# Kernel tuning notes

Measured on AMD Instinct MI355X. Metric: run time of the kernel, lower is better.

## Reference

```python
import jax, jax.numpy as jnp
import numpy as np

# Straight-through sign: forward = sign (with sign(0)=+1), backward = identity clipped to |x|<=1.
# Used both for weight binarization (BinaryLinearLayer) and StepActivationFunction.
@jax.custom_vjp
def ste_sign(x):
    return jnp.where(x >= 0, 1.0, -1.0).astype(x.dtype)

def _ste_fwd(x):
    return ste_sign(x), x

def _ste_bwd(x, g):
    return (g * (jnp.abs(x) <= 1.0).astype(g.dtype),)

ste_sign.defvjp(_ste_fwd, _ste_bwd)

def binary_linear(x, w):
    # BinaryLinearLayer: matmul against sign-binarized weights, no bias.
    return x @ ste_sign(w).T


def setup_inputs() -> dict:
    key = jax.random.key(0)
    ks = jax.random.split(key, 5)
    B = 65536
    x = jax.random.normal(ks[0], (B, 784), dtype=jnp.float32)
    w1 = jax.random.normal(ks[1], (256, 784), dtype=jnp.float32) * 0.1
    w2 = jax.random.normal(ks[2], (128, 256), dtype=jnp.float32) * 0.1
    w3 = jax.random.normal(ks[3], (32, 128), dtype=jnp.float32) * 0.1
    w4 = jax.random.normal(ks[4], (10, 32), dtype=jnp.float32) * 0.1
    return {"x": x, "w1": w1, "w2": w2, "w3": w3, "w4": w4}


def reference(x, w1, w2, w3, w4):
    h = x.reshape(-1, 28 * 28)                 # [B, 784]
    h = ste_sign(binary_linear(h, w1))         # [B, 256]
    h = ste_sign(binary_linear(h, w2))         # [B, 128]
    h = ste_sign(binary_linear(h, w3))         # [B, 32]
    return binary_linear(h, w4)                # [B, 10] logits, no final step
```

## Files before the change

### kernel.cpp

```cpp
#include <hip/hip_runtime.h>
#include <stdint.h>

typedef __bf16 bf16;
typedef bf16 bf16x8 __attribute__((ext_vector_type(8)));
typedef float f32x4 __attribute__((ext_vector_type(4)));

#define B_ROWS   65536
#define K1       784
#define CAPW     64
#define NWAVES   4096

#define CNT_OFF  0
#define LIST_OFF 16384
#define S1F_OFF  1064960
#define W2P_OFF  1474560
#define W3P_OFF  1478656
#define W4P_OFF  1479168
#define H1P_OFF  1479680

#define AS1C(p) ((const __attribute__((address_space(1))) void*)(p))
#define AS3(p)  ((__attribute__((address_space(3))) void*)(p))

__global__ __launch_bounds__(256) void prep_kernel(
    const float* __restrict__ w1, const float* __restrict__ w2,
    const float* __restrict__ w3, const float* __restrict__ w4,
    bf16* __restrict__ s1f, uint32_t* __restrict__ w2p,
    uint32_t* __restrict__ w3p, uint32_t* __restrict__ w4p) {
  int gid = blockIdx.x * 256 + threadIdx.x;
  {
    int j = gid & 7, l = (gid >> 3) & 63, t = (gid >> 9) & 15, s = gid >> 13;
    int fr = l & 15, fg = l >> 4;
    int n = t * 16 + fr;
    int k = s * 32 + fg * 8 + j;
    bf16 v = (bf16)0.0f;
    if (k < K1) v = (w1[n * K1 + k] >= 0.0f) ? (bf16)1.0f : (bf16)-1.0f;
    s1f[gid] = v;
  }
  if (gid < 1024) {
    int j = gid >> 3, w = gid & 7;
    uint32_t bits = 0;
    for (int i = 0; i < 32; ++i)
      bits |= (w2[j * 256 + w * 32 + i] >= 0.0f ? 1u : 0u) << i;
    w2p[gid] = bits;
  }
  if (gid < 128) {
    int j = gid >> 2, w = gid & 3;
    uint32_t bits = 0;
    for (int i = 0; i < 32; ++i)
      bits |= (w3[j * 128 + w * 32 + i] >= 0.0f ? 1u : 0u) << i;
    w3p[gid] = bits;
  }
  if (gid < 16) {
    uint32_t bits = 0;
    if (gid < 10)
      for (int i = 0; i < 32; ++i)
        bits |= (w4[gid * 32 + i] >= 0.0f ? 1u : 0u) << i;
    w4p[gid] = bits;
  }
}

__global__ __launch_bounds__(256, 4) void gemm1_kernel(
    const float* __restrict__ x, const bf16* __restrict__ s1f,
    uint8_t* __restrict__ h1b, uint32_t* __restrict__ cntArr,
    uint32_t* __restrict__ list) {
  __shared__ __align__(16) bf16 Bs[2][8192];

  const int tid = threadIdx.x;
  const int lane = tid & 63;
  const int wid = tid >> 6;
  const int fr = lane & 15, fg = lane >> 4;
  const int m0 = blockIdx.x * 64 + wid * 16;
  const int waveId = blockIdx.x * 4 + wid;

  f32x4 acc[16];
#pragma unroll
  for (int j = 0; j < 16; ++j) acc[j] = (f32x4){0.f, 0.f, 0.f, 0.f};

  const float* xp0 = x + (size_t)(m0 + fr) * K1 + fg * 8;

  float4 ar[2][2];

#define STAGE_B(buf_, t_)                                                      \
  {                                                                            \
    _Pragma("unroll") for (int c = 0; c < 4; ++c)                              \
        __builtin_amdgcn_global_load_lds(                                      \
            AS1C(s1f + ((size_t)(t_) * 16 + wid * 4 + c) * 512 + lane * 8),    \
            AS3(&Bs[buf_][(wid * 4 + c) * 512]), 16, 0, 0);                    \
  }

#define LOAD_A(par_, t_)                                                       \
  {                                                                            \
    ar[par_][0] = *(const float4*)(xp0 + (t_) * 32);                           \
    ar[par_][1] = *(const float4*)(xp0 + (t_) * 32 + 4);                       \
  }

#define LOAD_A24(par_)                                                         \
  {                                                                            \
    float4 z = make_float4(0.f, 0.f, 0.f, 0.f);                                \
    if (fg < 2) {                                                              \
      ar[par_][0] = *(const float4*)(xp0 + 24 * 32);                           \
      ar[par_][1] = *(const float4*)(xp0 + 24 * 32 + 4);                       \
    } else {                                                                   \
      ar[par_][0] = z; ar[par_][1] = z;                                        \
    }                                                                          \
  }

#define STEP(t_, cur_, nxt_, PF_)                                              \
  {                                                                            \
    if ((PF_) == 1) LOAD_A(nxt_, (t_) + 1)                                     \
    else if ((PF_) == 2) LOAD_A24(nxt_)                                        \
    if ((PF_) != 0) STAGE_B((cur_) ^ 1, (t_) + 1)                              \
    bf16x8 ah, al;                                                             \
    {                                                                          \
      float4 v0 = ar[cur_][0], v1 = ar[cur_][1];                               \
      bf16 h0 = (bf16)v0.x, h1 = (bf16)v0.y, h2 = (bf16)v0.z, h3 = (bf16)v0.w; \
      bf16 h4 = (bf16)v1.x, h5 = (bf16)v1.y, h6 = (bf16)v1.z, h7 = (bf16)v1.w; \
      bf16 l0 = (bf16)(v0.x - (float)h0), l1 = (bf16)(v0.y - (float)h1);       \
      bf16 l2 = (bf16)(v0.z - (float)h2), l3 = (bf16)(v0.w - (float)h3);       \
      bf16 l4 = (bf16)(v1.x - (float)h4), l5 = (bf16)(v1.y - (float)h5);       \
      bf16 l6 = (bf16)(v1.z - (float)h6), l7 = (bf16)(v1.w - (float)h7);       \
      ah = (bf16x8){h0, h1, h2, h3, h4, h5, h6, h7};                           \
      al = (bf16x8){l0, l1, l2, l3, l4, l5, l6, l7};                           \
    }                                                                          \
    _Pragma("unroll") for (int jg = 0; jg < 4; ++jg) {                         \
      bf16x8 b0 = *(const bf16x8*)&Bs[cur_][(jg * 4 + 0) * 512 + lane * 8];    \
      bf16x8 b1 = *(const bf16x8*)&Bs[cur_][(jg * 4 + 1) * 512 + lane * 8];    \
      bf16x8 b2 = *(const bf16x8*)&Bs[cur_][(jg * 4 + 2) * 512 + lane * 8];    \
      bf16x8 b3 = *(const bf16x8*)&Bs[cur_][(jg * 4 + 3) * 512 + lane * 8];    \
      acc[jg * 4 + 0] = __builtin_amdgcn_mfma_f32_16x16x32_bf16(ah, b0, acc[jg * 4 + 0], 0, 0, 0); \
      acc[jg * 4 + 0] = __builtin_amdgcn_mfma_f32_16x16x32_bf16(al, b0, acc[jg * 4 + 0], 0, 0, 0); \
      acc[jg * 4 + 1] = __builtin_amdgcn_mfma_f32_16x16x32_bf16(ah, b1, acc[jg * 4 + 1], 0, 0, 0); \
      acc[jg * 4 + 1] = __builtin_amdgcn_mfma_f32_16x16x32_bf16(al, b1, acc[jg * 4 + 1], 0, 0, 0); \
      acc[jg * 4 + 2] = __builtin_amdgcn_mfma_f32_16x16x32_bf16(ah, b2, acc[jg * 4 + 2], 0, 0, 0); \
      acc[jg * 4 + 2] = __builtin_amdgcn_mfma_f32_16x16x32_bf16(al, b2, acc[jg * 4 + 2], 0, 0, 0); \
      acc[jg * 4 + 3] = __builtin_amdgcn_mfma_f32_16x16x32_bf16(ah, b3, acc[jg * 4 + 3], 0, 0, 0); \
      acc[jg * 4 + 3] = __builtin_amdgcn_mfma_f32_16x16x32_bf16(al, b3, acc[jg * 4 + 3], 0, 0, 0); \
    }                                                                          \
    if ((PF_) != 0) __syncthreads();                                           \
  }

  STAGE_B(0, 0)
  LOAD_A(0, 0)
  __syncthreads();

  for (int tt = 0; tt < 11; ++tt) {
    STEP(2 * tt,     0, 1, 1)
    STEP(2 * tt + 1, 1, 0, 1)
  }
  STEP(22, 0, 1, 1)
  STEP(23, 1, 0, 2)
  STEP(24, 0, 0, 0)

  uint32_t* wlist = list + (size_t)waveId * CAPW;
  uint32_t wcnt = 0;

#define FLAG(v_, jj_, rr_)                                                     \
  {                                                                            \
    unsigned long long fb = __ballot(__builtin_fabsf(v_) < 0.05f);             \
    if (fb) {                                                                  \
      if (__builtin_fabsf(v_) < 0.05f) {                                       \
        uint32_t pos = wcnt + (uint32_t)__popcll(fb & ((1ull << lane) - 1ull));\
        if (pos < CAPW)                                                        \
          wlist[pos] = ((uint32_t)(m0 + fg * 4 + (rr_)) << 8) |                \
                       (uint32_t)((jj_) * 16 + fr);                            \
      }                                                                        \
      wcnt += (uint32_t)__popcll(fb);                                          \
    }                                                                          \
  }

#pragma unroll
  for (int r = 0; r < 4; ++r) {
    uint32_t w[8];
#pragma unroll
    for (int jp = 0; jp < 8; ++jp) {
      float v0 = acc[2 * jp][r];
      float v1 = acc[2 * jp + 1][r];
      unsigned long long s0 = __ballot(v0 >= 0.0f);
      unsigned long long s1 = __ballot(v1 >= 0.0f);
      FLAG(v0, 2 * jp, r)
      FLAG(v1, 2 * jp + 1, r)
      w[jp] = (uint32_t)((s0 >> (fg * 16)) & 0xFFFF) |
              ((uint32_t)((s1 >> (fg * 16)) & 0xFFFF) << 16);
    }
    if (fr == 0) {
      int m = m0 + fg * 4 + r;
      *(uint4*)(h1b + (size_t)m * 32)      = make_uint4(w[0], w[1], w[2], w[3]);
      *(uint4*)(h1b + (size_t)m * 32 + 16) = make_uint4(w[4], w[5], w[6], w[7]);
    }
  }

  if (lane == 0) cntArr[waveId] = (wcnt < CAPW) ? wcnt : CAPW;
}

__global__ __launch_bounds__(256) void cleanup_kernel(
    const float* __restrict__ x, const float* __restrict__ w1,
    uint32_t* __restrict__ h1p, const uint32_t* __restrict__ cntArr,
    const uint32_t* __restrict__ list) {
  for (uint32_t idx = blockIdx.x * 256 + threadIdx.x; idx < NWAVES * CAPW;
       idx += 65536) {
    uint32_t w = idx >> 6, li = idx & (CAPW - 1);
    if (li >= cntArr[w]) continue;
    uint32_t e = list[idx];
    uint32_t col = e & 255u, b = e >> 8;
    const float4* xr4 = (const float4*)(x + (size_t)b * K1);
    const float4* wr4 = (const float4*)(w1 + (size_t)col * K1);
    float t1 = 0.0f, t2 = 0.0f;
    for (int k4 = 0; k4 < 128; ++k4) {
      float4 xv = xr4[k4], wv = wr4[k4];
      t1 += (wv.x >= 0.f) ? xv.x : -xv.x;
      t1 += (wv.y >= 0.f) ? xv.y : -xv.y;
      t1 += (wv.z >= 0.f) ? xv.z : -xv.z;
      t1 += (wv.w >= 0.f) ? xv.w : -xv.w;
    }
    for (int k4 = 128; k4 < 196; ++k4) {
      float4 xv = xr4[k4], wv = wr4[k4];
      t2 += (wv.x >= 0.f) ? xv.x : -xv.x;
      t2 += (wv.y >= 0.f) ? xv.y : -xv.y;
      t2 += (wv.z >= 0.f) ? xv.z : -xv.z;
      t2 += (wv.w >= 0.f) ? xv.w : -xv.w;
    }
    float s = t1 + t2;
    uint32_t word = b * 8u + (col >> 5);
    uint32_t mask = 1u << (col & 31u);
    if (s >= 0.0f) atomicOr(&h1p[word], mask);
    else           atomicAnd(&h1p[word], ~mask);
  }
}

__global__ __launch_bounds__(256) void layer234_kernel(
    const uint32_t* __restrict__ h1p, const uint32_t* __restrict__ w2p,
    const uint32_t* __restrict__ w3p, const uint32_t* __restrict__ w4p,
    float* __restrict__ out) {
  __shared__ __align__(16) uint32_t lw[1168];
  for (int i = threadIdx.x; i < 1168; i += 256) {
    uint32_t v;
    if (i < 1024) v = w2p[i];
    else if (i < 1152) v = w3p[i - 1024];
    else v = w4p[i - 1152];
    lw[i] = v;
  }
  __syncthreads();
  int b = blockIdx.x * 256 + threadIdx.x;
  const uint4* hp = (const uint4*)h1p;
  uint4 a0 = hp[(size_t)b * 2], a1 = hp[(size_t)b * 2 + 1];

  uint32_t h2w[4] = {0u, 0u, 0u, 0u};
#pragma unroll 4
  for (int j = 0; j < 128; ++j) {
    uint4 w0 = *(const uint4*)&lw[j * 8];
    uint4 w1v = *(const uint4*)&lw[j * 8 + 4];
    int t = __popc(a0.x ^ w0.x) + __popc(a0.y ^ w0.y) +
            __popc(a0.z ^ w0.z) + __popc(a0.w ^ w0.w) +
            __popc(a1.x ^ w1v.x) + __popc(a1.y ^ w1v.y) +
            __popc(a1.z ^ w1v.z) + __popc(a1.w ^ w1v.w);
    h2w[j >> 5] |= (uint32_t)(t <= 128) << (j & 31);
  }
  uint32_t h3 = 0u;
#pragma unroll 4
  for (int j = 0; j < 32; ++j) {
    uint4 w0 = *(const uint4*)&lw[1024 + j * 4];
    int t = __popc(h2w[0] ^ w0.x) + __popc(h2w[1] ^ w0.y) +
            __popc(h2w[2] ^ w0.z) + __popc(h2w[3] ^ w0.w);
    h3 |= (uint32_t)(t <= 64) << j;
  }
  float* o = out + (size_t)b * 10;
#pragma unroll
  for (int c = 0; c < 10; ++c) {
    int t = __popc(h3 ^ lw[1152 + c]);
    o[c] = (float)(32 - 2 * t);
  }
}

extern "C" void kernel_launch(void* const* d_in, const int* in_sizes, int n_in,
                              void* d_out, int out_size, void* d_ws, size_t ws_size,
                              hipStream_t stream) {
  const float* x  = (const float*)d_in[0];
  const float* w1 = (const float*)d_in[1];
  const float* w2 = (const float*)d_in[2];
  const float* w3 = (const float*)d_in[3];
  const float* w4 = (const float*)d_in[4];
  float* out = (float*)d_out;
  uint8_t* ws = (uint8_t*)d_ws;

  uint32_t* cntArr = (uint32_t*)(ws + CNT_OFF);
  uint32_t* list   = (uint32_t*)(ws + LIST_OFF);
  bf16*     s1f    = (bf16*)(ws + S1F_OFF);
  uint32_t* w2p    = (uint32_t*)(ws + W2P_OFF);
  uint32_t* w3p    = (uint32_t*)(ws + W3P_OFF);
  uint32_t* w4p    = (uint32_t*)(ws + W4P_OFF);
  uint32_t* h1p    = (uint32_t*)(ws + H1P_OFF);

  prep_kernel<<<800, 256, 0, stream>>>(w1, w2, w3, w4, s1f, w2p, w3p, w4p);
  gemm1_kernel<<<1024, 256, 0, stream>>>(x, s1f, (uint8_t*)h1p, cntArr, list);
  cleanup_kernel<<<256, 256, 0, stream>>>(x, w1, h1p, cntArr, list);
  layer234_kernel<<<B_ROWS / 256, 256, 0, stream>>>(h1p, w2p, w3p, w4p, out);
}
```

Before: 428.3 us.

## Fuse first-layer GEMM, near-zero cleanup and binary layers 2-4 into one kernel

The separate cleanup and layer234 kernels are merged into the first-layer GEMM kernel. Each wave now keeps its 16 rows of layer-1 sign bits and its list of near-zero candidates in LDS. It recomputes those candidates exactly in-wave with LDS atomics, then runs the popcount layers 2-4 on 16 lanes and writes the logits directly. This removes two launches and the global round-trip of the bit-packed activations and flag lists. In exchange it adds LDS pressure to an occupancy-bound kernel, serial per-wave exact dot products, and popcount work that uses only a quarter of each wave. The per-wave flag capacity also drops from 64 to 48 entries.

Measured after the change: 375.4 us. 1.14x faster.

```diff
diff --git a/kernel.cpp b/kernel.cpp
--- a/kernel.cpp
+++ b/kernel.cpp
@@ -7,16 +7,11 @@
 
 #define B_ROWS   65536
 #define K1       784
-#define CAPW     64
-#define NWAVES   4096
-
-#define CNT_OFF  0
-#define LIST_OFF 16384
-#define S1F_OFF  1064960
-#define W2P_OFF  1474560
-#define W3P_OFF  1478656
-#define W4P_OFF  1479168
-#define H1P_OFF  1479680
+
+#define S1F_OFF  0
+#define W2P_OFF  409600
+#define W3P_OFF  413696
+#define W4P_OFF  414208
 
 #define AS1C(p) ((const __attribute__((address_space(1))) void*)(p))
 #define AS3(p)  ((__attribute__((address_space(3))) void*)(p))
@@ -59,18 +54,21 @@
   }
 }
 
-__global__ __launch_bounds__(256, 4) void gemm1_kernel(
+__global__ __launch_bounds__(256, 4) void fused_kernel(
     const float* __restrict__ x, const bf16* __restrict__ s1f,
-    uint8_t* __restrict__ h1b, uint32_t* __restrict__ cntArr,
-    uint32_t* __restrict__ list) {
+    const float* __restrict__ w1, const uint32_t* __restrict__ w2p,
+    const uint32_t* __restrict__ w3p, const uint32_t* __restrict__ w4p,
+    float* __restrict__ out) {
   __shared__ __align__(16) bf16 Bs[2][8192];
+  __shared__ __align__(16) uint32_t lw[1168];
+  __shared__ __align__(16) uint32_t h1w[4][16][8];
+  __shared__ uint32_t flg[4][48];
 
   const int tid = threadIdx.x;
   const int lane = tid & 63;
   const int wid = tid >> 6;
   const int fr = lane & 15, fg = lane >> 4;
   const int m0 = blockIdx.x * 64 + wid * 16;
-  const int waveId = blockIdx.x * 4 + wid;
 
   f32x4 acc[16];
 #pragma unroll
@@ -139,6 +137,13 @@
     if ((PF_) != 0) __syncthreads();                                           \
   }
 
+  for (int i = tid; i < 1168; i += 256) {
+    uint32_t v;
+    if (i < 1024) v = w2p[i];
+    else if (i < 1152) v = w3p[i - 1024];
+    else v = w4p[i - 1152];
+    lw[i] = v;
+  }
   STAGE_B(0, 0)
   LOAD_A(0, 0)
   __syncthreads();
@@ -151,8 +156,10 @@
   STEP(23, 1, 0, 2)
   STEP(24, 0, 0, 0)
 
-  uint32_t* wlist = list + (size_t)waveId * CAPW;
+  uint32_t* wflg = &flg[wid][0];
+  uint32_t* wh1  = &h1w[wid][0][0];
   uint32_t wcnt = 0;
+  const int myrow = lane & 15;
 
 #define FLAG(v_, jj_, rr_)                                                     \
   {                                                                            \
@@ -160,17 +167,17 @@
     if (fb) {                                                                  \
       if (__builtin_fabsf(v_) < 0.05f) {                                       \
         uint32_t pos = wcnt + (uint32_t)__popcll(fb & ((1ull << lane) - 1ull));\
-        if (pos < CAPW)                                                        \
-          wlist[pos] = ((uint32_t)(m0 + fg * 4 + (rr_)) << 8) |                \
-                       (uint32_t)((jj_) * 16 + fr);                            \
+        if (pos < 48)                                                          \
+          wflg[pos] = ((uint32_t)(fg * 4 + (rr_)) << 8) |                      \
+                      (uint32_t)((jj_) * 16 + fr);                             \
       }                                                                        \
       wcnt += (uint32_t)__popcll(fb);                                          \
     }                                                                          \
   }
 
+  uint32_t myw[8] = {0u, 0u, 0u, 0u, 0u, 0u, 0u, 0u};
 #pragma unroll
   for (int r = 0; r < 4; ++r) {
-    uint32_t w[8];
 #pragma unroll
     for (int jp = 0; jp < 8; ++jp) {
       float v0 = acc[2 * jp][r];
@@ -179,30 +186,22 @@
       unsigned long long s1 = __ballot(v1 >= 0.0f);
       FLAG(v0, 2 * jp, r)
       FLAG(v1, 2 * jp + 1, r)
-      w[jp] = (uint32_t)((s0 >> (fg * 16)) & 0xFFFF) |
-              ((uint32_t)((s1 >> (fg * 16)) & 0xFFFF) << 16);
-    }
-    if (fr == 0) {
-      int m = m0 + fg * 4 + r;
-      *(uint4*)(h1b + (size_t)m * 32)      = make_uint4(w[0], w[1], w[2], w[3]);
-      *(uint4*)(h1b + (size_t)m * 32 + 16) = make_uint4(w[4], w[5], w[6], w[7]);
-    }
-  }
-
-  if (lane == 0) cntArr[waveId] = (wcnt < CAPW) ? wcnt : CAPW;
-}
-
-__global__ __launch_bounds__(256) void cleanup_kernel(
-    const float* __restrict__ x, const float* __restrict__ w1,
-    uint32_t* __restrict__ h1p, const uint32_t* __restrict__ cntArr,
-    const uint32_t* __restrict__ list) {
-  for (uint32_t idx = blockIdx.x * 256 + threadIdx.x; idx < NWAVES * CAPW;
-       idx += 65536) {
-    uint32_t w = idx >> 6, li = idx & (CAPW - 1);
-    if (li >= cntArr[w]) continue;
-    uint32_t e = list[idx];
-    uint32_t col = e & 255u, b = e >> 8;
-    const float4* xr4 = (const float4*)(x + (size_t)b * K1);
+      uint32_t wv = (uint32_t)((s0 >> ((myrow >> 2) * 16)) & 0xFFFF) |
+                    ((uint32_t)((s1 >> ((myrow >> 2) * 16)) & 0xFFFF) << 16);
+      if ((myrow & 3) == r) myw[jp] = wv;
+    }
+  }
+  if (lane < 16) {
+    *(uint4*)&wh1[myrow * 8]     = make_uint4(myw[0], myw[1], myw[2], myw[3]);
+    *(uint4*)&wh1[myrow * 8 + 4] = make_uint4(myw[4], myw[5], myw[6], myw[7]);
+  }
+  asm volatile("s_waitcnt lgkmcnt(0)" ::: "memory");
+
+  uint32_t nf = (wcnt < 48) ? wcnt : 48;
+  if (lane < nf) {
+    uint32_t e = wflg[lane];
+    uint32_t col = e & 255u, mlocal = e >> 8;
+    const float4* xr4 = (const float4*)(x + (size_t)(m0 + mlocal) * K1);
     const float4* wr4 = (const float4*)(w1 + (size_t)col * K1);
     float t1 = 0.0f, t2 = 0.0f;
     for (int k4 = 0; k4 < 128; ++k4) {
@@ -220,54 +219,41 @@
       t2 += (wv.w >= 0.f) ? xv.w : -xv.w;
     }
     float s = t1 + t2;
-    uint32_t word = b * 8u + (col >> 5);
+    uint32_t word = mlocal * 8u + (col >> 5);
     uint32_t mask = 1u << (col & 31u);
-    if (s >= 0.0f) atomicOr(&h1p[word], mask);
-    else           atomicAnd(&h1p[word], ~mask);
-  }
-}
-
-__global__ __launch_bounds__(256) void layer234_kernel(
-    const uint32_t* __restrict__ h1p, const uint32_t* __restrict__ w2p,
-    const uint32_t* __restrict__ w3p, const uint32_t* __restrict__ w4p,
-    float* __restrict__ out) {
-  __shared__ __align__(16) uint32_t lw[1168];
-  for (int i = threadIdx.x; i < 1168; i += 256) {
-    uint32_t v;
-    if (i < 1024) v = w2p[i];
-    else if (i < 1152) v = w3p[i - 1024];
-    else v = w4p[i - 1152];
-    lw[i] = v;
-  }
-  __syncthreads();
-  int b = blockIdx.x * 256 + threadIdx.x;
-  const uint4* hp = (const uint4*)h1p;
-  uint4 a0 = hp[(size_t)b * 2], a1 = hp[(size_t)b * 2 + 1];
-
-  uint32_t h2w[4] = {0u, 0u, 0u, 0u};
+    if (s >= 0.0f) atomicOr((unsigned int*)&wh1[word], mask);
+    else           atomicAnd((unsigned int*)&wh1[word], ~mask);
+  }
+  asm volatile("s_waitcnt vmcnt(0) lgkmcnt(0)" ::: "memory");
+
+  if (lane < 16) {
+    uint4 a0 = *(const uint4*)&wh1[myrow * 8];
+    uint4 a1 = *(const uint4*)&wh1[myrow * 8 + 4];
+    uint32_t h2w[4] = {0u, 0u, 0u, 0u};
 #pragma unroll 4
-  for (int j = 0; j < 128; ++j) {
-    uint4 w0 = *(const uint4*)&lw[j * 8];
-    uint4 w1v = *(const uint4*)&lw[j * 8 + 4];
-    int t = __popc(a0.x ^ w0.x) + __popc(a0.y ^ w0.y) +
-            __popc(a0.z ^ w0.z) + __popc(a0.w ^ w0.w) +
-            __popc(a1.x ^ w1v.x) + __popc(a1.y ^ w1v.y) +
-            __popc(a1.z ^ w1v.z) + __popc(a1.w ^ w1v.w);
-    h2w[j >> 5] |= (uint32_t)(t <= 128) << (j & 31);
-  }
-  uint32_t h3 = 0u;
+    for (int j = 0; j < 128; ++j) {
+      uint4 w0 = *(const uint4*)&lw[j * 8];
+      uint4 w1v = *(const uint4*)&lw[j * 8 + 4];
+      int t = __popc(a0.x ^ w0.x) + __popc(a0.y ^ w0.y) +
+              __popc(a0.z ^ w0.z) + __popc(a0.w ^ w0.w) +
+              __popc(a1.x ^ w1v.x) + __popc(a1.y ^ w1v.y) +
+              __popc(a1.z ^ w1v.z) + __popc(a1.w ^ w1v.w);
+      h2w[j >> 5] |= (uint32_t)(t <= 128) << (j & 31);
+    }
+    uint32_t h3 = 0u;
 #pragma unroll 4
-  for (int j = 0; j < 32; ++j) {
-    uint4 w0 = *(const uint4*)&lw[1024 + j * 4];
-    int t = __popc(h2w[0] ^ w0.x) + __popc(h2w[1] ^ w0.y) +
-            __popc(h2w[2] ^ w0.z) + __popc(h2w[3] ^ w0.w);
-    h3 |= (uint32_t)(t <= 64) << j;
-  }
-  float* o = out + (size_t)b * 10;
-#pragma unroll
-  for (int c = 0; c < 10; ++c) {
-    int t = __popc(h3 ^ lw[1152 + c]);
-    o[c] = (float)(32 - 2 * t);
+    for (int j = 0; j < 32; ++j) {
+      uint4 w0 = *(const uint4*)&lw[1024 + j * 4];
+      int t = __popc(h2w[0] ^ w0.x) + __popc(h2w[1] ^ w0.y) +
+              __popc(h2w[2] ^ w0.z) + __popc(h2w[3] ^ w0.w);
+      h3 |= (uint32_t)(t <= 64) << j;
+    }
+    float* o = out + (size_t)(m0 + myrow) * 10;
+#pragma unroll
+    for (int c = 0; c < 10; ++c) {
+      int t = __popc(h3 ^ lw[1152 + c]);
+      o[c] = (float)(32 - 2 * t);
+    }
   }
 }
 
@@ -282,16 +268,11 @@
   float* out = (float*)d_out;
   uint8_t* ws = (uint8_t*)d_ws;
 
-  uint32_t* cntArr = (uint32_t*)(ws + CNT_OFF);
-  uint32_t* list   = (uint32_t*)(ws + LIST_OFF);
-  bf16*     s1f    = (bf16*)(ws + S1F_OFF);
-  uint32_t* w2p    = (uint32_t*)(ws + W2P_OFF);
-  uint32_t* w3p    = (uint32_t*)(ws + W3P_OFF);
-  uint32_t* w4p    = (uint32_t*)(ws + W4P_OFF);
-  uint32_t* h1p    = (uint32_t*)(ws + H1P_OFF);
+  bf16*     s1f = (bf16*)(ws + S1F_OFF);
+  uint32_t* w2p = (uint32_t*)(ws + W2P_OFF);
+  uint32_t* w3p = (uint32_t*)(ws + W3P_OFF);
+  uint32_t* w4p = (uint32_t*)(ws + W4P_OFF);
 
   prep_kernel<<<800, 256, 0, stream>>>(w1, w2, w3, w4, s1f, w2p, w3p, w4p);
-  gemm1_kernel<<<1024, 256, 0, stream>>>(x, s1f, (uint8_t*)h1p, cntArr, list);
-  cleanup_kernel<<<256, 256, 0, stream>>>(x, w1, h1p, cntArr, list);
-  layer234_kernel<<<B_ROWS / 256, 256, 0, stream>>>(h1p, w2p, w3p, w4p, out);
+  fused_kernel<<<1024, 256, 0, stream>>>(x, s1f, w1, w2p, w3p, w4p, out);
 }
```
